# Performance work log

Measured on AMD Instinct MI355X. Metric: run time of the kernel, lower is better.

Reference implementation:

```python
import math
import jax, jax.numpy as jnp
import numpy as np

H = 1024        # hidden_size
NH = 16         # num_attention_heads
HD = H // NH    # attention_head_size
I = 4096        # intermediate_size
B, S = 4, 2048
LN_EPS = 1e-5


def setup_inputs() -> dict:
    key = jax.random.key(0)
    ks = jax.random.split(key, 12)
    s = 0.02
    return {
        "x": jax.random.normal(ks[0], (B, S, H), dtype=jnp.float32),
        "ln1_g": jnp.ones((H,), jnp.float32),
        "ln1_b": jnp.zeros((H,), jnp.float32),
        "qkv_w": jax.random.normal(ks[1], (H, 3 * H), jnp.float32) * s,
        "qkv_b": jnp.zeros((3 * H,), jnp.float32),
        "out_w": jax.random.normal(ks[2], (H, H), jnp.float32) * s,
        "out_b": jnp.zeros((H,), jnp.float32),
        "ln2_g": jnp.ones((H,), jnp.float32),
        "ln2_b": jnp.zeros((H,), jnp.float32),
        "w1": jax.random.normal(ks[3], (H, I), jnp.float32) * s,
        "b1": jnp.zeros((I,), jnp.float32),
        "w2": jax.random.normal(ks[4], (I, H), jnp.float32) * s,
        "b2": jnp.zeros((H,), jnp.float32),
    }


def _layernorm(x, g, b):
    mu = jnp.mean(x, axis=-1, keepdims=True)
    var = jnp.mean(jnp.square(x - mu), axis=-1, keepdims=True)
    return (x - mu) * jax.lax.rsqrt(var + LN_EPS) * g + b


def _gelu_tanh(x):
    c = math.sqrt(2.0 / math.pi)
    return 0.5 * x * (1.0 + jnp.tanh(c * (x + 0.044715 * x * x * x)))


def reference(x, ln1_g, ln1_b, qkv_w, qkv_b, out_w, out_b, ln2_g, ln2_b, w1, b1, w2, b2):
    b, s, _ = x.shape
    h = _layernorm(x, ln1_g, ln1_b)
    qkv = h @ qkv_w + qkv_b                      # [B,S,3H]
    q, k, v = jnp.split(qkv, 3, axis=-1)
    # [B,S,H] -> [B,NH,S,HD]
    def heads(t):
        return t.reshape(b, s, NH, HD).transpose(0, 2, 1, 3)
    q, k, v = heads(q), heads(k), heads(v)
    scores = jnp.einsum("bhqd,bhkd->bhqk", q, k) / math.sqrt(HD)
    probs = jax.nn.softmax(scores, axis=-1)
    attn = jnp.einsum("bhqk,bhkd->bhqd", probs, v)
    attn = attn.transpose(0, 2, 1, 3).reshape(b, s, H)
    attn = attn @ out_w + out_b
    x = x + attn
    h2 = _layernorm(x, ln2_g, ln2_b)
    mlp = _gelu_tanh(h2 @ w1 + b1) @ w2 + b2
    x = x + mlp
    return x
```

## Files before the change

kernel.cpp:

```cpp
#include <hip/hip_runtime.h>
#include <math.h>

#define H 1024
#define NHEAD 16
#define HDIM 64
#define IDIM 4096
#define BATCH 4
#define SEQ 2048
#define NTOK 8192
#define LN_EPS 1e-5f

#define QK_EXP2_SCALE 0.18033688011112042f

typedef __bf16 bf16x8 __attribute__((ext_vector_type(8)));
typedef __bf16 bf16x4 __attribute__((ext_vector_type(4)));
typedef float f32x4 __attribute__((ext_vector_type(4)));
typedef unsigned short ushort8 __attribute__((ext_vector_type(8)));
typedef unsigned short ushort4v __attribute__((ext_vector_type(4)));

__device__ __forceinline__ unsigned short f2bf(float f) {
  union { float f; unsigned int u; } v; v.f = f;
  unsigned int u = v.u;
  return (unsigned short)((u + 0x7FFFu + ((u >> 16) & 1u)) >> 16);
}

__global__ void transpose_cast_all(const float* __restrict__ W0, unsigned short* __restrict__ T0,
                                   const float* __restrict__ W1, unsigned short* __restrict__ T1,
                                   const float* __restrict__ W2, unsigned short* __restrict__ T2,
                                   const float* __restrict__ W3, unsigned short* __restrict__ T3) {
  __shared__ unsigned short tile[32][33];
  int bid = blockIdx.x;
  const float* W;
  unsigned short* Wt;
  int K, N, ntx, local;
  if (bid < 3072) {
    W = W0; Wt = T0; K = H; N = 3 * H; ntx = 3 * H / 32; local = bid;
  } else if (bid < 4096) {
    W = W1; Wt = T1; K = H; N = H; ntx = H / 32; local = bid - 3072;
  } else if (bid < 8192) {
    W = W2; Wt = T2; K = H; N = IDIM; ntx = IDIM / 32; local = bid - 4096;
  } else {
    W = W3; Wt = T3; K = IDIM; N = H; ntx = H / 32; local = bid - 8192;
  }
  int n0 = (local % ntx) * 32, k0 = (local / ntx) * 32;
  int tx = threadIdx.x, ty = threadIdx.y;
#pragma unroll
  for (int i = 0; i < 4; i++) {
    int k = ty + i * 8;
    tile[tx][k] = f2bf(W[(size_t)(k0 + k) * N + n0 + tx]);
  }
  __syncthreads();
#pragma unroll
  for (int i = 0; i < 4; i++) {
    int n = ty + i * 8;
    Wt[(size_t)(n0 + n) * K + k0 + tx] = tile[n][tx];
  }
}

__global__ __launch_bounds__(256)
void layernorm_kernel(const float* __restrict__ x, const float* __restrict__ g,
                      const float* __restrict__ b, unsigned short* __restrict__ out) {
  __shared__ float sb[4];
  int row = blockIdx.x;
  int tid = threadIdx.x;
  const float4* xr = (const float4*)(x + (size_t)row * H);
  float4 v = xr[tid];
  float s = v.x + v.y + v.z + v.w;
#pragma unroll
  for (int o = 32; o > 0; o >>= 1) s += __shfl_down(s, o);
  if ((tid & 63) == 0) sb[tid >> 6] = s;
  __syncthreads();
  float mu = (sb[0] + sb[1] + sb[2] + sb[3]) * (1.0f / H);
  __syncthreads();
  float dx = v.x - mu, dy = v.y - mu, dz = v.z - mu, dw = v.w - mu;
  float s2 = dx * dx + dy * dy + dz * dz + dw * dw;
#pragma unroll
  for (int o = 32; o > 0; o >>= 1) s2 += __shfl_down(s2, o);
  if ((tid & 63) == 0) sb[tid >> 6] = s2;
  __syncthreads();
  float var = (sb[0] + sb[1] + sb[2] + sb[3]) * (1.0f / H);
  float rs = rsqrtf(var + LN_EPS);
  float4 gv = ((const float4*)g)[tid];
  float4 bv = ((const float4*)b)[tid];
  ushort4v ov;
  ov[0] = f2bf(dx * rs * gv.x + bv.x);
  ov[1] = f2bf(dy * rs * gv.y + bv.y);
  ov[2] = f2bf(dz * rs * gv.z + bv.z);
  ov[3] = f2bf(dw * rs * gv.w + bv.w);
  ((ushort4v*)(out + (size_t)row * H))[tid] = ov;
}

template <int EPI>
__global__ __launch_bounds__(256)
void gemm_bt_kernel(const unsigned short* __restrict__ A,
                    const unsigned short* __restrict__ Bt,
                    const float* __restrict__ bias,
                    const float* __restrict__ res,
                    void* __restrict__ out, unsigned short* __restrict__ vt_out,
                    int M, int N, int K) {
  __shared__ __align__(16) unsigned short As[2][128 * 32];
  __shared__ __align__(16) unsigned short Bs[2][128 * 32];
  int tid = threadIdx.x;
  int wave = tid >> 6, lane = tid & 63;
  int quad = lane >> 4, l16 = lane & 15;
  int wm = wave >> 1, wn = wave & 1;
  int m0 = blockIdx.y * 128, n0 = blockIdx.x * 128;
  f32x4 acc[4][4];
#pragma unroll
  for (int i = 0; i < 4; i++)
#pragma unroll
    for (int j = 0; j < 4; j++) acc[i][j] = (f32x4){0.f, 0.f, 0.f, 0.f};

  int rl = (lane >> 2);
  int cphys = lane & 3;

  auto stage = [&](int k0, int sel) {
#pragma unroll
    for (int t = 0; t < 2; t++) {
      int ch = wave * 2 + t;
      int rloc = ch * 16 + rl;
      int clog = cphys ^ ((rloc >> 1) & 3);
      const unsigned short* ga = A + (size_t)(m0 + rloc) * K + k0 + clog * 8;
      __builtin_amdgcn_global_load_lds(
          (const __attribute__((address_space(1))) unsigned int*)ga,
          (__attribute__((address_space(3))) unsigned int*)(&As[sel][ch * 512]), 16, 0, 0);
      const unsigned short* gb = Bt + (size_t)(n0 + rloc) * K + k0 + clog * 8;
      __builtin_amdgcn_global_load_lds(
          (const __attribute__((address_space(1))) unsigned int*)gb,
          (__attribute__((address_space(3))) unsigned int*)(&Bs[sel][ch * 512]), 16, 0, 0);
    }
  };

  stage(0, 0);
  for (int k0 = 0; k0 < K; k0 += 32) {
    int sel = (k0 >> 5) & 1;
    __syncthreads();
    if (k0 + 32 < K) stage(k0 + 32, sel ^ 1);
    bf16x8 af[4], bfv[4];
#pragma unroll
    for (int i = 0; i < 4; i++) {
      int ra = wm * 64 + i * 16 + l16;
      af[i] = *(const bf16x8*)&As[sel][ra * 32 + ((quad ^ ((ra >> 1) & 3)) << 3)];
      int rb = wn * 64 + i * 16 + l16;
      bfv[i] = *(const bf16x8*)&Bs[sel][rb * 32 + ((quad ^ ((rb >> 1) & 3)) << 3)];
    }
#pragma unroll
    for (int i = 0; i < 4; i++)
#pragma unroll
      for (int j = 0; j < 4; j++)
        acc[i][j] = __builtin_amdgcn_mfma_f32_16x16x32_bf16(bfv[j], af[i], acc[i][j], 0, 0, 0);
  }
#pragma unroll
  for (int i = 0; i < 4; i++) {
    int m = m0 + wm * 64 + i * 16 + l16;
#pragma unroll
    for (int j = 0; j < 4; j++) {
      int nb = n0 + wn * 64 + j * 16 + quad * 4;
      float4 bv4 = *(const float4*)&bias[nb];
      float v0 = acc[i][j][0] + bv4.x;
      float v1 = acc[i][j][1] + bv4.y;
      float v2 = acc[i][j][2] + bv4.z;
      float v3 = acc[i][j][3] + bv4.w;
      size_t off = (size_t)m * N + nb;
      float4 rv = *(const float4*)&res[off];
      float4 o4;
      o4.x = v0 + rv.x; o4.y = v1 + rv.y; o4.z = v2 + rv.z; o4.w = v3 + rv.w;
      *(float4*)&((float*)out)[off] = o4;
    }
  }
}

template <int EPI>
__global__ __launch_bounds__(512, 2)
void gemm256_kernel(const unsigned short* __restrict__ A,
                    const unsigned short* __restrict__ Bt,
                    const float* __restrict__ bias,
                    void* __restrict__ out, unsigned short* __restrict__ vt_out,
                    int M, int N, int K) {
  __shared__ __align__(16) unsigned short As[2][256 * 64];
  __shared__ __align__(16) unsigned short Bs[2][256 * 64];
  int tid = threadIdx.x;
  int wave = tid >> 6, lane = tid & 63;
  int quad = lane >> 4, l16 = lane & 15;
  int wm = wave >> 2, wn = wave & 3;
  int nwg = gridDim.x * gridDim.y;
  int dlin = blockIdx.y * gridDim.x + blockIdx.x;
  int swz = (dlin & 7) * (nwg >> 3) + (dlin >> 3);
  int nm = gridDim.y;
  int mt = swz % nm, nt = swz / nm;
  int m0 = mt * 256, n0 = nt * 256;
  int NT = K >> 6;

  const unsigned short* Abase = A + (size_t)m0 * K;
  const unsigned short* Bbase = Bt + (size_t)n0 * K;

  int srow = lane >> 3;
  int schunk = (lane & 7) ^ srow;

  auto stage = [&](const unsigned short* gbase, unsigned short* lbase, int tile,
                   int half) {
    int kt = tile < NT ? tile : NT - 1;
    int k0 = kt << 6;
    unsigned short* lb = lbase + (size_t)(tile & 1) * (256 * 64);
#pragma unroll
    for (int L = 0; L < 2; L++) {
      int rloc = half * 128 + L * 64 + wave * 8 + srow;
      const unsigned short* g = gbase + (size_t)rloc * K + k0 + schunk * 8;
      __builtin_amdgcn_global_load_lds(
          (const __attribute__((address_space(1))) unsigned int*)g,
          (__attribute__((address_space(3))) unsigned int*)(lb + (size_t)(half * 128 + L * 64 + wave * 8) * 64),
          16, 0, 0);
    }
  };

  f32x4 acc[8][4];
#pragma unroll
  for (int i = 0; i < 8; i++)
#pragma unroll
    for (int j = 0; j < 4; j++) acc[i][j] = (f32x4){0.f, 0.f, 0.f, 0.f};
  bf16x8 af[4][2];
  bf16x8 bv[4][2];

  stage(Abase, (unsigned short*)As, 0, 0);
  stage(Bbase, (unsigned short*)Bs, 0, 0);
  stage(Abase, (unsigned short*)As, 0, 1);
  stage(Bbase, (unsigned short*)Bs, 0, 1);
  stage(Abase, (unsigned short*)As, 1, 0);
  stage(Bbase, (unsigned short*)Bs, 1, 0);
  stage(Abase, (unsigned short*)As, 1, 1);
  stage(Bbase, (unsigned short*)Bs, 1, 1);
  asm volatile("s_waitcnt vmcnt(8)" ::: "memory");
  __builtin_amdgcn_s_barrier();

  for (int it = 0; it < (NT >> 1); it++) {
    int t = it * 2;
#pragma unroll
    for (int P = 0; P < 8; P++) {
      int ct = t + (P >> 2);
      int sel = ct & 1;
      if ((P & 3) == 0) {
#pragma unroll
        for (int i = 0; i < 4; i++) {
          int ra = wm * 128 + i * 16 + l16;
#pragma unroll
          for (int ks = 0; ks < 2; ks++)
            af[i][ks] = *(const bf16x8*)&As[sel][ra * 64 + (((ks * 4 + quad) ^ (ra & 7)) << 3)];
        }
#pragma unroll
        for (int j = 0; j < 2; j++) {
          int rb = wn * 64 + j * 16 + l16;
#pragma unroll
          for (int ks = 0; ks < 2; ks++)
            bv[j][ks] = *(const bf16x8*)&Bs[sel][rb * 64 + (((ks * 4 + quad) ^ (rb & 7)) << 3)];
        }
      } else if ((P & 3) == 1) {
#pragma unroll
        for (int j = 0; j < 2; j++) {
          int rb = wn * 64 + (2 + j) * 16 + l16;
#pragma unroll
          for (int ks = 0; ks < 2; ks++)
            bv[2 + j][ks] = *(const bf16x8*)&Bs[sel][rb * 64 + (((ks * 4 + quad) ^ (rb & 7)) << 3)];
        }
      } else if ((P & 3) == 2) {
#pragma unroll
        for (int i = 0; i < 4; i++) {
          int ra = wm * 128 + (4 + i) * 16 + l16;
#pragma unroll
          for (int ks = 0; ks < 2; ks++)
            af[i][ks] = *(const bf16x8*)&As[sel][ra * 64 + (((ks * 4 + quad) ^ (ra & 7)) << 3)];
        }
      }
      switch (P) {
        case 2: stage(Bbase, (unsigned short*)Bs, t + 2, 0); break;
        case 3: stage(Abase, (unsigned short*)As, t + 2, 0);
                stage(Bbase, (unsigned short*)Bs, t + 2, 1); break;
        case 4: stage(Abase, (unsigned short*)As, t + 2, 1); break;
        case 6: stage(Bbase, (unsigned short*)Bs, t + 3, 0);
                stage(Bbase, (unsigned short*)Bs, t + 3, 1); break;
        case 7: stage(Abase, (unsigned short*)As, t + 3, 0);
                stage(Abase, (unsigned short*)As, t + 3, 1); break;
        default: break;
      }
      __builtin_amdgcn_s_barrier();
      int qm = (P >> 1) & 1, qj = P & 1;
      __builtin_amdgcn_s_setprio(1);
#pragma unroll
      for (int i = 0; i < 4; i++)
#pragma unroll
        for (int j = 0; j < 2; j++)
#pragma unroll
          for (int ks = 0; ks < 2; ks++)
            acc[qm * 4 + i][qj * 2 + j] = __builtin_amdgcn_mfma_f32_16x16x32_bf16(
                bv[qj * 2 + j][ks], af[i][ks], acc[qm * 4 + i][qj * 2 + j], 0, 0, 0);
      __builtin_amdgcn_s_setprio(0);
      if (P == 3) asm volatile("s_waitcnt vmcnt(6)" ::: "memory");
      if (P == 7) asm volatile("s_waitcnt vmcnt(8)" ::: "memory");
      __builtin_amdgcn_s_barrier();
    }
  }
  asm volatile("s_waitcnt vmcnt(0)" ::: "memory");

  bool vslice = (EPI == 0) && (vt_out != nullptr) && (n0 >= 2 * H);
#pragma unroll
  for (int i = 0; i < 8; i++) {
    int m = m0 + wm * 128 + i * 16 + l16;
#pragma unroll
    for (int j = 0; j < 4; j++) {
      int nb = n0 + wn * 64 + j * 16 + quad * 4;
      float4 bv4 = *(const float4*)&bias[nb];
      float v0 = acc[i][j][0] + bv4.x;
      float v1 = acc[i][j][1] + bv4.y;
      float v2 = acc[i][j][2] + bv4.z;
      float v3 = acc[i][j][3] + bv4.w;
      size_t off = (size_t)m * N + nb;
      if (EPI == 0) {
        if (vslice) {
          int bb = m >> 11, s = m & (SEQ - 1);
          int cb = nb - 2 * H;
          int hh = cb >> 6, dd = cb & 63;
          size_t base = ((size_t)(bb * NHEAD + hh) * HDIM + dd) * SEQ + s;
          vt_out[base] = f2bf(v0);
          vt_out[base + SEQ] = f2bf(v1);
          vt_out[base + 2 * SEQ] = f2bf(v2);
          vt_out[base + 3 * SEQ] = f2bf(v3);
        } else {
          if (n0 < H) {
            v0 *= QK_EXP2_SCALE; v1 *= QK_EXP2_SCALE;
            v2 *= QK_EXP2_SCALE; v3 *= QK_EXP2_SCALE;
          }
          bf16x4 pk = {(__bf16)v0, (__bf16)v1, (__bf16)v2, (__bf16)v3};
          *(bf16x4*)&((unsigned short*)out)[off] = pk;
        }
      } else {
        float g0 = v0 / (1.f + __expf(-1.5957691216057308f * (v0 + 0.044715f * v0 * v0 * v0)));
        float g1 = v1 / (1.f + __expf(-1.5957691216057308f * (v1 + 0.044715f * v1 * v1 * v1)));
        float g2 = v2 / (1.f + __expf(-1.5957691216057308f * (v2 + 0.044715f * v2 * v2 * v2)));
        float g3 = v3 / (1.f + __expf(-1.5957691216057308f * (v3 + 0.044715f * v3 * v3 * v3)));
        bf16x4 pk = {(__bf16)g0, (__bf16)g1, (__bf16)g2, (__bf16)g3};
        *(bf16x4*)&((unsigned short*)out)[off] = pk;
      }
    }
  }
}

__global__ __launch_bounds__(512, 4)
void flash_attn_kernel(const unsigned short* __restrict__ qkv,
                       const unsigned short* __restrict__ vt,
                       unsigned short* __restrict__ attn_out) {
  constexpr int LPs = 40;
  __shared__ __align__(16) unsigned short Ks[2][64 * 64];
  __shared__ __align__(16) unsigned short Ps[8 * 32 * LPs];
  int tid = threadIdx.x;
  int wave = tid >> 6, lane = tid & 63;
  int quad = lane >> 4, l16 = lane & 15;
  int d = blockIdx.x;
  int logical = (d & 7) * 64 + (d >> 3);
  int bh = logical >> 3, qi = logical & 7;
  int b = bh >> 4, h = bh & 15;
  int qblk = qi * 256 + wave * 32;
  const size_t qrow = 3 * H;
  const size_t tok0 = (size_t)b * SEQ;
  const size_t vbase = (size_t)bh * HDIM * SEQ;
  unsigned short* Psw = Ps + wave * 32 * LPs;

  bf16x8 qb[2][2];
#pragma unroll
  for (int mb = 0; mb < 2; mb++)
#pragma unroll
    for (int ks = 0; ks < 2; ks++)
      qb[mb][ks] = *(const bf16x8*)&qkv[(tok0 + qblk + mb * 16 + l16) * qrow +
                                        h * HDIM + ks * 32 + quad * 8];

  float l_part[2] = {0.f, 0.f};
  f32x4 o_acc[2][4];
#pragma unroll
  for (int mb = 0; mb < 2; mb++)
#pragma unroll
    for (int db = 0; db < 4; db++) o_acc[mb][db] = (f32x4){0.f, 0.f, 0.f, 0.f};

  int srow = lane >> 3;
  int schunk = (lane & 7) ^ srow;

  {
    const unsigned short* ga =
        &qkv[(tok0 + wave * 8 + srow) * qrow + H + h * HDIM + schunk * 8];
    __builtin_amdgcn_global_load_lds(
        (const __attribute__((address_space(1))) unsigned int*)ga,
        (__attribute__((address_space(3))) unsigned int*)(&Ks[0][wave * 8 * 64]), 16, 0, 0);
  }

  for (int kv0 = 0; kv0 < SEQ; kv0 += 64) {
    int buf = (kv0 >> 6) & 1;
    const unsigned short* Kb = Ks[buf];
    unsigned short* Kn = Ks[buf ^ 1];
    __syncthreads();
    bf16x8 va[4];
#pragma unroll
    for (int db = 0; db < 4; db++)
      va[db] = *(const bf16x8*)&vt[vbase + (size_t)(db * 16 + l16) * SEQ +
                                   kv0 + quad * 8];
    if (kv0 + 64 < SEQ) {
      const unsigned short* ga =
          &qkv[(tok0 + kv0 + 64 + wave * 8 + srow) * qrow + H + h * HDIM + schunk * 8];
      __builtin_amdgcn_global_load_lds(
          (const __attribute__((address_space(1))) unsigned int*)ga,
          (__attribute__((address_space(3))) unsigned int*)(Kn + wave * 8 * 64), 16, 0, 0);
    }
#pragma unroll
    for (int half = 0; half < 2; half++) {
#pragma unroll
      for (int nbl = 0; nbl < 2; nbl++) {
        int nb = half * 2 + nbl;
        int row = nb * 16 + l16;
        bf16x8 ka[2];
#pragma unroll
        for (int ks = 0; ks < 2; ks++) {
          int pc = (ks * 4 + quad) ^ (row & 7);
          ka[ks] = *(const bf16x8*)&Kb[row * 64 + pc * 8];
        }
        f32x4 st[2];
#pragma unroll
        for (int mb = 0; mb < 2; mb++) st[mb] = (f32x4){0.f, 0.f, 0.f, 0.f};
        __builtin_amdgcn_s_setprio(1);
#pragma unroll
        for (int ks = 0; ks < 2; ks++)
#pragma unroll
          for (int mb = 0; mb < 2; mb++)
            st[mb] = __builtin_amdgcn_mfma_f32_16x16x32_bf16(ka[ks], qb[mb][ks], st[mb], 0, 0, 0);
        __builtin_amdgcn_s_setprio(0);
#pragma unroll
        for (int mb = 0; mb < 2; mb++) {
          float p0, p1, p2, p3;
          asm("v_exp_f32 %0, %1" : "=v"(p0) : "v"(st[mb][0]));
          asm("v_exp_f32 %0, %1" : "=v"(p1) : "v"(st[mb][1]));
          asm("v_exp_f32 %0, %1" : "=v"(p2) : "v"(st[mb][2]));
          asm("v_exp_f32 %0, %1" : "=v"(p3) : "v"(st[mb][3]));
          l_part[mb] += (p0 + p1) + (p2 + p3);
          bf16x4 pk = {(__bf16)p0, (__bf16)p1, (__bf16)p2, (__bf16)p3};
          *(bf16x4*)&Psw[(mb * 16 + l16) * LPs + nb * 16 + quad * 4] = pk;
        }
      }
      __asm__ volatile("s_waitcnt lgkmcnt(0)" ::: "memory");
      bf16x8 pb[2];
#pragma unroll
      for (int mb = 0; mb < 2; mb++)
        pb[mb] = *(const bf16x8*)&Psw[(mb * 16 + l16) * LPs + half * 32 + quad * 8];
      __builtin_amdgcn_s_setprio(1);
#pragma unroll
      for (int db = 0; db < 4; db++)
#pragma unroll
        for (int mb = 0; mb < 2; mb++)
          o_acc[mb][db] = __builtin_amdgcn_mfma_f32_16x16x32_bf16(va[db], pb[mb],
                                                                  o_acc[mb][db], 0, 0, 0);
      __builtin_amdgcn_s_setprio(0);
      if (half == 0) {
#pragma unroll
        for (int db = 0; db < 4; db++)
          va[db] = *(const bf16x8*)&vt[vbase + (size_t)(db * 16 + l16) * SEQ +
                                       kv0 + 32 + quad * 8];
      }
    }
  }
#pragma unroll
  for (int mb = 0; mb < 2; mb++) {
    l_part[mb] += __shfl_xor(l_part[mb], 16);
    l_part[mb] += __shfl_xor(l_part[mb], 32);
    l_part[mb] = 1.0f / l_part[mb];
  }
#pragma unroll
  for (int mb = 0; mb < 2; mb++) {
#pragma unroll
    for (int db = 0; db < 4; db++) {
      ushort4v o;
#pragma unroll
      for (int r = 0; r < 4; r++) o[r] = f2bf(o_acc[mb][db][r] * l_part[mb]);
      *(ushort4v*)&attn_out[(tok0 + qblk + mb * 16 + l16) * H + h * HDIM +
                            db * 16 + quad * 4] = o;
    }
  }
}

extern "C" void kernel_launch(void* const* d_in, const int* in_sizes, int n_in,
                              void* d_out, int out_size, void* d_ws, size_t ws_size,
                              hipStream_t stream) {
  const float* x = (const float*)d_in[0];
  const float* ln1_g = (const float*)d_in[1];
  const float* ln1_b = (const float*)d_in[2];
  const float* qkv_w = (const float*)d_in[3];
  const float* qkv_b = (const float*)d_in[4];
  const float* out_w = (const float*)d_in[5];
  const float* out_b = (const float*)d_in[6];
  const float* ln2_g = (const float*)d_in[7];
  const float* ln2_b = (const float*)d_in[8];
  const float* w1 = (const float*)d_in[9];
  const float* b1 = (const float*)d_in[10];
  const float* w2 = (const float*)d_in[11];
  const float* b2 = (const float*)d_in[12];
  float* outp = (float*)d_out;

  size_t off = 0;
  auto take = [&](size_t n) {
    char* p = (char*)d_ws + off;
    off += (n + 255) & ~(size_t)255;
    return p;
  };
  unsigned short* h1 = (unsigned short*)take((size_t)NTOK * H * 2);
  unsigned short* qkvb = (unsigned short*)take((size_t)NTOK * 3 * H * 2);
  unsigned short* attn = (unsigned short*)take((size_t)NTOK * H * 2);
  float* x1 = (float*)take((size_t)NTOK * H * 4);
  unsigned short* qkvwt = (unsigned short*)take((size_t)3 * H * H * 2);
  unsigned short* outwt = (unsigned short*)take((size_t)H * H * 2);
  unsigned short* w1t = (unsigned short*)take((size_t)H * IDIM * 2);
  unsigned short* w2t = (unsigned short*)take((size_t)H * IDIM * 2);
  unsigned short* h2 = h1;
  unsigned short* mid = qkvb;
  unsigned short* vt = (unsigned short*)x1;

  dim3 tb(32, 8);
  transpose_cast_all<<<dim3(12288), tb, 0, stream>>>(qkv_w, qkvwt, out_w, outwt,
                                                     w1, w1t, w2, w2t);

  layernorm_kernel<<<NTOK, 256, 0, stream>>>(x, ln1_g, ln1_b, h1);
  gemm256_kernel<0><<<dim3(3 * H / 256, NTOK / 256), 512, 0, stream>>>(
      h1, qkvwt, qkv_b, qkvb, vt, NTOK, 3 * H, H);
  flash_attn_kernel<<<dim3(SEQ / 256 * BATCH * NHEAD), 512, 0, stream>>>(qkvb, vt, attn);
  gemm_bt_kernel<2><<<dim3(H / 128, NTOK / 128), 256, 0, stream>>>(
      attn, outwt, out_b, x, x1, nullptr, NTOK, H, H);
  layernorm_kernel<<<NTOK, 256, 0, stream>>>(x1, ln2_g, ln2_b, h2);
  gemm256_kernel<1><<<dim3(IDIM / 256, NTOK / 256), 512, 0, stream>>>(
      h2, w1t, b1, mid, nullptr, NTOK, IDIM, H);
  gemm_bt_kernel<2><<<dim3(H / 128, NTOK / 128), 256, 0, stream>>>(
      mid, w2t, b2, x1, outp, nullptr, NTOK, H, IDIM);
}
```

Measured before the change: 600.8 us.

## Split-K 256x256 GEMM for MLP down-projection plus tile swizzle in 128 GEMM

```diff
diff --git a/kernel.cpp b/kernel.cpp
--- a/kernel.cpp
+++ b/kernel.cpp
@@ -104,7 +104,11 @@
   int wave = tid >> 6, lane = tid & 63;
   int quad = lane >> 4, l16 = lane & 15;
   int wm = wave >> 1, wn = wave & 1;
-  int m0 = blockIdx.y * 128, n0 = blockIdx.x * 128;
+  int nwg = gridDim.x * gridDim.y;
+  int dlin = blockIdx.y * gridDim.x + blockIdx.x;
+  int swz = (nwg & 7) ? dlin : ((dlin & 7) * (nwg >> 3) + (dlin >> 3));
+  int mt = swz / gridDim.x, nt = swz % gridDim.x;
+  int m0 = mt * 128, n0 = nt * 128;
   f32x4 acc[4][4];
 #pragma unroll
   for (int i = 0; i < 4; i++)
@@ -343,6 +347,167 @@
   }
 }
 
+__global__ __launch_bounds__(512, 2)
+void gemm256_sk_kernel(const unsigned short* __restrict__ A,
+                       const unsigned short* __restrict__ Bt,
+                       float* __restrict__ opart,
+                       int M, int N, int Kf, int KL) {
+  __shared__ __align__(16) unsigned short As[2][256 * 64];
+  __shared__ __align__(16) unsigned short Bs[2][256 * 64];
+  int tid = threadIdx.x;
+  int wave = tid >> 6, lane = tid & 63;
+  int quad = lane >> 4, l16 = lane & 15;
+  int wm = wave >> 2, wn = wave & 3;
+  int d = blockIdx.x;
+  int swz = (d & 7) * 32 + (d >> 3);
+  int sp = swz >> 7;
+  int rem = swz & 127;
+  int mt = rem >> 2, nt = rem & 3;
+  int m0 = mt * 256, n0 = nt * 256;
+  int NT = KL >> 6;
+  int k0g = sp * KL;
+
+  const unsigned short* Abase = A + (size_t)m0 * Kf + k0g;
+  const unsigned short* Bbase = Bt + (size_t)n0 * Kf + k0g;
+
+  int srow = lane >> 3;
+  int schunk = (lane & 7) ^ srow;
+
+  auto stage = [&](const unsigned short* gbase, unsigned short* lbase, int tile,
+                   int half) {
+    int kt = tile < NT ? tile : NT - 1;
+    int k0 = kt << 6;
+    unsigned short* lb = lbase + (size_t)(tile & 1) * (256 * 64);
+#pragma unroll
+    for (int L = 0; L < 2; L++) {
+      int rloc = half * 128 + L * 64 + wave * 8 + srow;
+      const unsigned short* g = gbase + (size_t)rloc * Kf + k0 + schunk * 8;
+      __builtin_amdgcn_global_load_lds(
+          (const __attribute__((address_space(1))) unsigned int*)g,
+          (__attribute__((address_space(3))) unsigned int*)(lb + (size_t)(half * 128 + L * 64 + wave * 8) * 64),
+          16, 0, 0);
+    }
+  };
+
+  f32x4 acc[8][4];
+#pragma unroll
+  for (int i = 0; i < 8; i++)
+#pragma unroll
+    for (int j = 0; j < 4; j++) acc[i][j] = (f32x4){0.f, 0.f, 0.f, 0.f};
+  bf16x8 af[4][2];
+  bf16x8 bv[4][2];
+
+  stage(Abase, (unsigned short*)As, 0, 0);
+  stage(Bbase, (unsigned short*)Bs, 0, 0);
+  stage(Abase, (unsigned short*)As, 0, 1);
+  stage(Bbase, (unsigned short*)Bs, 0, 1);
+  stage(Abase, (unsigned short*)As, 1, 0);
+  stage(Bbase, (unsigned short*)Bs, 1, 0);
+  stage(Abase, (unsigned short*)As, 1, 1);
+  stage(Bbase, (unsigned short*)Bs, 1, 1);
+  asm volatile("s_waitcnt vmcnt(8)" ::: "memory");
+  __builtin_amdgcn_s_barrier();
+
+  for (int it = 0; it < (NT >> 1); it++) {
+    int t = it * 2;
+#pragma unroll
+    for (int P = 0; P < 8; P++) {
+      int ct = t + (P >> 2);
+      int sel = ct & 1;
+      if ((P & 3) == 0) {
+#pragma unroll
+        for (int i = 0; i < 4; i++) {
+          int ra = wm * 128 + i * 16 + l16;
+#pragma unroll
+          for (int ks = 0; ks < 2; ks++)
+            af[i][ks] = *(const bf16x8*)&As[sel][ra * 64 + (((ks * 4 + quad) ^ (ra & 7)) << 3)];
+        }
+#pragma unroll
+        for (int j = 0; j < 2; j++) {
+          int rb = wn * 64 + j * 16 + l16;
+#pragma unroll
+          for (int ks = 0; ks < 2; ks++)
+            bv[j][ks] = *(const bf16x8*)&Bs[sel][rb * 64 + (((ks * 4 + quad) ^ (rb & 7)) << 3)];
+        }
+      } else if ((P & 3) == 1) {
+#pragma unroll
+        for (int j = 0; j < 2; j++) {
+          int rb = wn * 64 + (2 + j) * 16 + l16;
+#pragma unroll
+          for (int ks = 0; ks < 2; ks++)
+            bv[2 + j][ks] = *(const bf16x8*)&Bs[sel][rb * 64 + (((ks * 4 + quad) ^ (rb & 7)) << 3)];
+        }
+      } else if ((P & 3) == 2) {
+#pragma unroll
+        for (int i = 0; i < 4; i++) {
+          int ra = wm * 128 + (4 + i) * 16 + l16;
+#pragma unroll
+          for (int ks = 0; ks < 2; ks++)
+            af[i][ks] = *(const bf16x8*)&As[sel][ra * 64 + (((ks * 4 + quad) ^ (ra & 7)) << 3)];
+        }
+      }
+      switch (P) {
+        case 2: stage(Bbase, (unsigned short*)Bs, t + 2, 0); break;
+        case 3: stage(Abase, (unsigned short*)As, t + 2, 0);
+                stage(Bbase, (unsigned short*)Bs, t + 2, 1); break;
+        case 4: stage(Abase, (unsigned short*)As, t + 2, 1); break;
+        case 6: stage(Bbase, (unsigned short*)Bs, t + 3, 0);
+                stage(Bbase, (unsigned short*)Bs, t + 3, 1); break;
+        case 7: stage(Abase, (unsigned short*)As, t + 3, 0);
+                stage(Abase, (unsigned short*)As, t + 3, 1); break;
+        default: break;
+      }
+      __builtin_amdgcn_s_barrier();
+      int qm = (P >> 1) & 1, qj = P & 1;
+      __builtin_amdgcn_s_setprio(1);
+#pragma unroll
+      for (int i = 0; i < 4; i++)
+#pragma unroll
+        for (int j = 0; j < 2; j++)
+#pragma unroll
+          for (int ks = 0; ks < 2; ks++)
+            acc[qm * 4 + i][qj * 2 + j] = __builtin_amdgcn_mfma_f32_16x16x32_bf16(
+                bv[qj * 2 + j][ks], af[i][ks], acc[qm * 4 + i][qj * 2 + j], 0, 0, 0);
+      __builtin_amdgcn_s_setprio(0);
+      if (P == 3) asm volatile("s_waitcnt vmcnt(6)" ::: "memory");
+      if (P == 7) asm volatile("s_waitcnt vmcnt(8)" ::: "memory");
+      __builtin_amdgcn_s_barrier();
+    }
+  }
+  asm volatile("s_waitcnt vmcnt(0)" ::: "memory");
+
+  float* op = opart + (size_t)sp * M * N;
+#pragma unroll
+  for (int i = 0; i < 8; i++) {
+    int m = m0 + wm * 128 + i * 16 + l16;
+#pragma unroll
+    for (int j = 0; j < 4; j++) {
+      int nb = n0 + wn * 64 + j * 16 + quad * 4;
+      *(f32x4*)&op[(size_t)m * N + nb] = acc[i][j];
+    }
+  }
+}
+
+__global__ __launch_bounds__(256)
+void mlp2_combine_kernel(const float* __restrict__ p,
+                         const float* __restrict__ bias,
+                         const float* __restrict__ res,
+                         float* __restrict__ out) {
+  size_t tok = blockIdx.x;
+  int d4 = threadIdx.x * 4;
+  size_t off = tok * H + d4;
+  float4 a = *(const float4*)&p[off];
+  float4 c = *(const float4*)&p[(size_t)NTOK * H + off];
+  float4 bb = *(const float4*)&bias[d4];
+  float4 rv = *(const float4*)&res[off];
+  float4 o4;
+  o4.x = a.x + c.x + bb.x + rv.x;
+  o4.y = a.y + c.y + bb.y + rv.y;
+  o4.z = a.z + c.z + bb.z + rv.z;
+  o4.w = a.w + c.w + bb.w + rv.w;
+  *(float4*)&out[off] = o4;
+}
+
 __global__ __launch_bounds__(512, 4)
 void flash_attn_kernel(const unsigned short* __restrict__ qkv,
                        const unsigned short* __restrict__ vt,
@@ -512,6 +677,8 @@
   unsigned short* outwt = (unsigned short*)take((size_t)H * H * 2);
   unsigned short* w1t = (unsigned short*)take((size_t)H * IDIM * 2);
   unsigned short* w2t = (unsigned short*)take((size_t)H * IDIM * 2);
+  float* ppart = (float*)take((size_t)2 * NTOK * H * 4);
+  bool use_sk = off <= ws_size;
   unsigned short* h2 = h1;
   unsigned short* mid = qkvb;
   unsigned short* vt = (unsigned short*)x1;
@@ -529,6 +696,11 @@
   layernorm_kernel<<<NTOK, 256, 0, stream>>>(x1, ln2_g, ln2_b, h2);
   gemm256_kernel<1><<<dim3(IDIM / 256, NTOK / 256), 512, 0, stream>>>(
       h2, w1t, b1, mid, nullptr, NTOK, IDIM, H);
-  gemm_bt_kernel<2><<<dim3(H / 128, NTOK / 128), 256, 0, stream>>>(
-      mid, w2t, b2, x1, outp, nullptr, NTOK, H, IDIM);
-}
+  if (use_sk) {
+    gemm256_sk_kernel<<<dim3(256), 512, 0, stream>>>(mid, w2t, ppart, NTOK, H, IDIM, IDIM / 2);
+    mlp2_combine_kernel<<<dim3(NTOK), 256, 0, stream>>>(ppart, b2, x1, outp);
+  } else {
+    gemm_bt_kernel<2><<<dim3(H / 128, NTOK / 128), 256, 0, stream>>>(
+        mid, w2t, b2, x1, outp, nullptr, NTOK, H, IDIM);
+  }
+}
```

Result: faster. 579.4 us (-3.6%).
